# Optimization experiments

Hardware: AMD Instinct MI355X
Metric: run time of the kernel (lower is better)

## Reference

```python
import jax, jax.numpy as jnp
import numpy as np

# dims: G groups, A authors/group, P posts/author, DIN token-pooled feat, DEMB sentence-BERT dim
G, A, P, DIN, DEMB, HP, HA = 16, 64, 32, 768, 384, 256, 128


def setup_inputs() -> dict:
    key = jax.random.key(0)
    ks = jax.random.split(key, 8)
    s = lambda k, shape, scale: (jax.random.normal(k, shape, jnp.float32) * scale)
    return {
        "x": jax.random.normal(ks[0], (G, A, P, DIN), jnp.float32),
        "w_embed": s(ks[1], (DIN, DEMB), 0.02),   # BERT pooled-projection stand-in
        "b_embed": jnp.zeros((DEMB,), jnp.float32),
        "k_post": s(ks[2], (DEMB, 4 * HP), 0.05),  # Keras LSTM kernel, gates [i|f|c|o]
        "r_post": s(ks[3], (HP, 4 * HP), 0.05),    # recurrent kernel
        "b_post": jnp.zeros((4 * HP,), jnp.float32),
        "k_auth": s(ks[4], (HP, 4 * HA), 0.05),
        "r_auth": s(ks[5], (HA, 4 * HA), 0.05),
        "b_auth": jnp.zeros((4 * HA,), jnp.float32),
    }


def _lstm(x, Wk, Wr, b):
    """Keras-style LSTM, returns final hidden state. x: [B,T,D] -> [B,H]."""
    B = x.shape[0]
    H = Wr.shape[0]
    # precompute input projections for all timesteps in one GEMM: [T,B,4H]
    z = jnp.einsum('btd,dh->tbh', x, Wk) + b

    def step(carry, zt):
        h, c = carry
        g = zt + h @ Wr
        i, f, gg, o = jnp.split(g, 4, axis=-1)  # Keras gate order i,f,c,o
        c = jax.nn.sigmoid(f) * c + jax.nn.sigmoid(i) * jnp.tanh(gg)
        h = jax.nn.sigmoid(o) * jnp.tanh(c)
        return (h, c), None

    h0 = jnp.zeros((B, H), x.dtype)
    (h, _), _ = jax.lax.scan(step, (h0, h0), z)
    return h


def reference(x, w_embed, b_embed, k_post, r_post, b_post, k_auth, r_auth, b_auth):
    g, a, p, _ = x.shape
    # sentence embedding per post (BERT stand-in): [G,A,P,DEMB]
    e = jnp.einsum('gapd,de->gape', x, w_embed) + b_embed
    # LSTM over posts, batched across all (group, author) pairs: [G,A,HP]
    h_post = _lstm(e.reshape(g * a, p, e.shape[-1]), k_post, r_post, b_post)
    h_post = h_post.reshape(g, a, -1)
    # LSTM over authors: [G,HA]
    return _lstm(h_post, k_auth, r_auth, b_auth)
```

## Files before the change

kernel.cpp:

```cpp
#include <hip/hip_runtime.h>
#include <cstdint>
#include <cstddef>

#define G_    16
#define A_    64
#define P_    32
#define DIN_  768
#define DEMB_ 384
#define HP_   256
#define HA_   128
#define GA_   1024
#define N1_   1024
#define N2_   512
#define TCH   16

typedef float    f32x4   __attribute__((ext_vector_type(4)));
typedef _Float16 half8_t __attribute__((ext_vector_type(8)));
typedef _Float16 half4_t __attribute__((ext_vector_type(4)));

__device__ __forceinline__ float sigmoidf_(float x) { return 1.0f / (1.0f + __expf(-x)); }
__device__ __forceinline__ float tanhf_(float x) { return 2.0f / (1.0f + __expf(-2.0f * x)) - 1.0f; }
__device__ __forceinline__ _Float16 us2h(unsigned short u) { _Float16 h; __builtin_memcpy(&h, &u, 2); return h; }
__device__ __forceinline__ unsigned short h2us(_Float16 h) { unsigned short u; __builtin_memcpy(&u, &h, 2); return u; }


__global__ __launch_bounds__(256) void k_wk(const float* __restrict__ w_embed,
                                            const float* __restrict__ k_post,
                                            float* __restrict__ Bmat) {
    int j  = blockIdx.x * 256 + threadIdx.x;
    int k0 = blockIdx.y * 4;
    float acc0 = 0.f, acc1 = 0.f, acc2 = 0.f, acc3 = 0.f;
    for (int d = 0; d < DEMB_; ++d) {
        float kp = k_post[(size_t)d * N1_ + j];
        acc0 += w_embed[(size_t)(k0 + 0) * DEMB_ + d] * kp;
        acc1 += w_embed[(size_t)(k0 + 1) * DEMB_ + d] * kp;
        acc2 += w_embed[(size_t)(k0 + 2) * DEMB_ + d] * kp;
        acc3 += w_embed[(size_t)(k0 + 3) * DEMB_ + d] * kp;
    }
    Bmat[(size_t)(k0 + 0) * N1_ + j] = acc0;
    Bmat[(size_t)(k0 + 1) * N1_ + j] = acc1;
    Bmat[(size_t)(k0 + 2) * N1_ + j] = acc2;
    Bmat[(size_t)(k0 + 3) * N1_ + j] = acc3;
}

__global__ __launch_bounds__(256) void k_bias_p(const float* __restrict__ b_embed,
                                                const float* __restrict__ k_post,
                                                const float* __restrict__ b_post,
                                                float* __restrict__ biasZp) {
    int p = blockIdx.x * 256 + threadIdx.x;
    int n = (p >> 6) * 16 + (p & 15) + 256 * ((p >> 4) & 3);
    float acc = b_post[n];
    for (int d = 0; d < DEMB_; ++d)
        acc += b_embed[d] * k_post[(size_t)d * N1_ + n];
    biasZp[p] = acc;
}

__global__ __launch_bounds__(256) void k_t16(const float* __restrict__ Bmat,
                                             _Float16* __restrict__ Bt16) {
    __shared__ float tile[64][65];
    const int tid = threadIdx.x;
    const int p0 = blockIdx.x * 64;
    const int k0 = blockIdx.y * 64;
    const int jgrp = p0 >> 6;
#pragma unroll
    for (int i = 0; i < 16; ++i) {
        int idx = i * 256 + tid;
        int pp = idx & 63, kk = idx >> 6;
        int n = jgrp * 16 + (pp & 15) + 256 * ((pp >> 4) & 3);
        tile[pp][kk] = Bmat[(size_t)(k0 + kk) * N1_ + n];
    }
    __syncthreads();
    const int pp = tid >> 2;
    const int kq = (tid & 3) * 16;
    _Float16 buf[16];
#pragma unroll
    for (int i = 0; i < 16; ++i) buf[i] = (_Float16)tile[pp][kq + i];
    _Float16* dst = &Bt16[(size_t)(p0 + pp) * DIN_ + k0 + kq];
    *(half8_t*)dst       = *(half8_t*)&buf[0];
    *(half8_t*)(dst + 8) = *(half8_t*)&buf[8];
}

__global__ __launch_bounds__(256) void k_bfrag(const float* __restrict__ r_post,
                                               _Float16* __restrict__ Bfrag) {
    int idx = blockIdx.x * 256 + threadIdx.x;
    int pt = idx >> 9;
    int kt = (idx >> 6) & 7;
    int l  = idx & 63;
    int p = pt * 16 + (l & 15);
    int n = (p >> 6) * 16 + (p & 15) + 256 * ((p >> 4) & 3);
    int kb = kt * 32 + (l >> 4) * 8;
    _Float16 buf[8];
#pragma unroll
    for (int s = 0; s < 8; ++s) buf[s] = (_Float16)r_post[(size_t)(kb + s) * N1_ + n];
    *(half8_t*)&Bfrag[(size_t)idx * 8] = *(half8_t*)buf;
}

#define ZBM 128
#define ZBN 256
#define ZBK 32
#define ZPAD 40

struct ZgLDS {
    union {
        struct { _Float16 As[ZBM][ZPAD]; _Float16 Bs[ZBN][ZPAD]; } S;
        _Float16 Hs[64][264];
    } u;
};
struct RecLDS {
    _Float16 wlds[16 * 8 * 64 * 8];
    _Float16 hbuf[2][4096];
};

__device__ __forceinline__ void zgemm_core(ZgLDS* L, int bid, int tid,
                                           const float* __restrict__ x,
                                           const _Float16* __restrict__ Bt16,
                                           const float* __restrict__ biasZp,
                                           _Float16* __restrict__ Zq, int tbase) {
    const int wg = (bid & 7) * 64 + (bid >> 3);
    const int bm = (wg & 127) * ZBM;
    const int bn = (wg >> 7) * ZBN;

    const int arow = tid >> 3, akq = (tid & 7) * 4;
    const int brow = tid >> 2, bkq = (tid & 3) * 8;
    const int lane = tid & 63, w = tid >> 6;
    const int wm = (w >> 2) * 32, wn = (w & 3) * 64;
    const int frc = lane & 15, frk = (lane >> 4) * 8;

    const int crow = bm + arow;
    const size_t xrow = (size_t)(crow >> 4) * P_ + tbase + (crow & 15);
    const float*    aptr = &x[xrow * DIN_ + akq];
    const _Float16* bptr = &Bt16[(size_t)(bn + brow) * DIN_ + bkq];

    f32x4 acc[2][4];
#pragma unroll
    for (int i = 0; i < 2; ++i)
#pragma unroll
        for (int j = 0; j < 4; ++j) acc[i][j] = (f32x4)0.0f;

    float4 a0 = *(const float4*)aptr;
    uint4  b0 = *(const uint4*)bptr;

    const int NK = DIN_ / ZBK;
    for (int kt = 0; kt < NK; ++kt) {
        const int kn = (kt + 1 < NK) ? (kt + 1) * ZBK : kt * ZBK;
        float4 na0 = *(const float4*)(aptr + kn);
        uint4  nb0 = *(const uint4*)(bptr + kn);

        half4_t ahv;
        ahv[0] = (_Float16)a0.x; ahv[1] = (_Float16)a0.y;
        ahv[2] = (_Float16)a0.z; ahv[3] = (_Float16)a0.w;

        __syncthreads();
        *(half4_t*)&L->u.S.As[arow][akq] = ahv;
        *(uint4*)&L->u.S.Bs[brow][bkq]   = b0;
        __syncthreads();

        half8_t bf[4];
#pragma unroll
        for (int fn = 0; fn < 4; ++fn)
            bf[fn] = *(const half8_t*)&L->u.S.Bs[wn + fn * 16 + frc][frk];
#pragma unroll
        for (int fm = 0; fm < 2; ++fm) {
            half8_t aH = *(const half8_t*)&L->u.S.As[wm + fm * 16 + frc][frk];
#pragma unroll
            for (int fn = 0; fn < 4; ++fn)
                acc[fm][fn] = __builtin_amdgcn_mfma_f32_16x16x32_f16(aH, bf[fn], acc[fm][fn], 0, 0, 0);
        }
        a0 = na0; b0 = nb0;
    }

    float bzv[4];
#pragma unroll
    for (int fn = 0; fn < 4; ++fn) bzv[fn] = biasZp[bn + wn + fn * 16 + frc];

#pragma unroll
    for (int half_ = 0; half_ < 2; ++half_) {
        __syncthreads();
        if ((w >> 3) == half_) {
#pragma unroll
            for (int fm = 0; fm < 2; ++fm)
#pragma unroll
                for (int fn = 0; fn < 4; ++fn)
#pragma unroll
                    for (int r = 0; r < 4; ++r) {
                        int rl = ((w >> 2) & 1) * 32 + fm * 16 + (lane >> 4) * 4 + r;
                        int cl = wn + fn * 16 + frc;
                        int clp = ((cl >> 6) * 16 + (cl & 15)) * 4 + ((cl >> 4) & 3);
                        L->u.Hs[rl][clp] = (_Float16)(acc[fm][fn][r] + bzv[fn]);
                    }
        }
        __syncthreads();
        const int brb = (bm + half_ * 64) >> 4;
        const int rg  = brb >> 4;
        const int l4r = (brb & 15) >> 2;
        {
            int tloc = tid >> 6, hcl = tid & 63;
            _Float16 buf[16];
#pragma unroll
            for (int rr = 0; rr < 4; ++rr) {
                half4_t h4 = *(const half4_t*)&L->u.Hs[tloc + 16 * rr][hcl * 4];
                buf[rr * 4 + 0] = h4[0]; buf[rr * 4 + 1] = h4[1];
                buf[rr * 4 + 2] = h4[2]; buf[rr * 4 + 3] = h4[3];
            }
            int wvg  = (bn >> 6) + (hcl >> 4);
            int tid2 = wvg * 64 + l4r * 16 + (hcl & 15);
            _Float16* dst = &Zq[((size_t)(tloc * 64 + rg) * 1024 + tid2) * 16];
            *(uint4*)dst       = *(const uint4*)&buf[0];
            *(uint4*)(dst + 8) = *(const uint4*)&buf[8];
        }
    }
}

__device__ __forceinline__ void rec_core(RecLDS* L, int blk, int tid,
                                         const _Float16* __restrict__ Zq,
                                         const _Float16* __restrict__ Bfrag,
                                         float* __restrict__ csave,
                                         unsigned short* __restrict__ hsave,
                                         float* __restrict__ hF32, int tbase) {
    const int lane = tid & 63, wv = tid >> 6;
    const int hl = lane & 15, l4 = lane >> 4;
    const int r0 = blk * 16;
    const int hc = wv * 16 + hl;

    half8_t wreg[16];
#pragma unroll
    for (int q = 0; q < 2; ++q)
#pragma unroll
        for (int kt = 0; kt < 8; ++kt)
            wreg[q * 8 + kt] = *(const half8_t*)&Bfrag[(((size_t)(4 * wv + q) * 8 + kt) * 64 + lane) * 8];
#pragma unroll
    for (int kt = 0; kt < 8; ++kt)
        *(half8_t*)&L->wlds[((wv * 8 + kt) * 64 + lane) * 8] =
            *(const half8_t*)&Bfrag[(((size_t)(4 * wv + 2) * 8 + kt) * 64 + lane) * 8];
    const _Float16* w3base = &Bfrag[((size_t)(4 * wv + 3) * 8 * 64 + lane) * 8];

    float cst[4];
    if (tbase == 0) {
#pragma unroll
        for (int i = 0; i < 4; ++i) cst[i] = 0.f;
    } else {
        f32x4 cv = *(const f32x4*)&csave[((size_t)blk * 1024 + tid) * 4];
#pragma unroll
        for (int i = 0; i < 4; ++i) cst[i] = cv[i];
#pragma unroll
        for (int rr = 0; rr < 4; ++rr) {
            int row = l4 * 4 + rr;
            int lidx = (((hc >> 5) * 64) + (((hc & 31) >> 3) * 16 + row)) * 8 + (hc & 7);
            L->hbuf[0][lidx] = us2h(hsave[((size_t)(r0 + row)) * HP_ + hc]);
        }
    }
    __syncthreads();

    const _Float16* zp0 = &Zq[((size_t)blk * 1024 + tid) * 16];
    half8_t z01N = *(const half8_t*)zp0;
    half8_t z23N = *(const half8_t*)(zp0 + 8);

    for (int tt = 0; tt < TCH; ++tt) {
        const int t = tbase + tt;
        const int cur = t & 1, nxt = cur ^ 1;

        half8_t z01 = z01N, z23 = z23N;
        if (tt + 1 < TCH) {
            const _Float16* zpn = zp0 + (size_t)(tt + 1) * 1048576;
            z01N = *(const half8_t*)zpn;
            z23N = *(const half8_t*)(zpn + 8);
        }

        f32x4 acc[4];
#pragma unroll
        for (int i = 0; i < 4; ++i) acc[i] = (f32x4)0.0f;

        if (t > 0) {
#pragma unroll
            for (int kt = 0; kt < 8; ++kt) {
                half8_t ah = *(const half8_t*)&L->hbuf[cur][(kt * 64 + lane) * 8];
                half8_t b2 = *(const half8_t*)&L->wlds[((wv * 8 + kt) * 64 + lane) * 8];
                half8_t w3 = *(const half8_t*)&w3base[(size_t)kt * 512];
                acc[0] = __builtin_amdgcn_mfma_f32_16x16x32_f16(ah, wreg[kt],     acc[0], 0, 0, 0);
                acc[1] = __builtin_amdgcn_mfma_f32_16x16x32_f16(ah, wreg[8 + kt], acc[1], 0, 0, 0);
                acc[2] = __builtin_amdgcn_mfma_f32_16x16x32_f16(ah, b2,           acc[2], 0, 0, 0);
                acc[3] = __builtin_amdgcn_mfma_f32_16x16x32_f16(ah, w3,           acc[3], 0, 0, 0);
            }
        }

        const bool last = (t == P_ - 1);
        const bool save = (tbase == 0) && (tt == TCH - 1);
#pragma unroll
        for (int rr = 0; rr < 4; ++rr) {
            const half8_t zsrc = (rr < 2) ? z01 : z23;
            const int o = (rr & 1) * 4;
            float gi = acc[0][rr] + (float)zsrc[o + 0];
            float gf = acc[1][rr] + (float)zsrc[o + 1];
            float gg = acc[2][rr] + (float)zsrc[o + 2];
            float go = acc[3][rr] + (float)zsrc[o + 3];
            float cn = sigmoidf_(gf) * cst[rr] + sigmoidf_(gi) * tanhf_(gg);
            cst[rr] = cn;
            float hv = sigmoidf_(go) * tanhf_(cn);
            int row = l4 * 4 + rr;
            int lidx = (((hc >> 5) * 64) + (((hc & 31) >> 3) * 16 + row)) * 8 + (hc & 7);
            _Float16 hh = (_Float16)hv;
            L->hbuf[nxt][lidx] = hh;
            if (save) hsave[((size_t)(r0 + row)) * HP_ + hc] = h2us(hh);
            if (last) hF32[(size_t)(r0 + row) * HP_ + hc] = hv;
        }
        __syncthreads();
    }

    if (tbase == 0) {
        f32x4 cv;
#pragma unroll
        for (int i = 0; i < 4; ++i) cv[i] = cst[i];
        *(f32x4*)&csave[((size_t)blk * 1024 + tid) * 4] = cv;
    }
}

__global__ __launch_bounds__(1024, 4) void k_zgemm(const float* __restrict__ x,
                                                   const _Float16* __restrict__ Bt16,
                                                   const float* __restrict__ biasZp,
                                                   _Float16* __restrict__ Zq, int tbase) {
    __shared__ __align__(16) ZgLDS L;
    zgemm_core(&L, blockIdx.x, threadIdx.x, x, Bt16, biasZp, Zq, tbase);
}

__global__ __launch_bounds__(1024, 4) void k_rec(const _Float16* __restrict__ Zq,
                                                 const _Float16* __restrict__ Bfrag,
                                                 float* __restrict__ csave,
                                                 unsigned short* __restrict__ hsave,
                                                 float* __restrict__ hF32, int tbase) {
    __shared__ __align__(16) RecLDS L;
    rec_core(&L, blockIdx.x, threadIdx.x, Zq, Bfrag, csave, hsave, hF32, tbase);
}

__global__ __launch_bounds__(1024, 4) void k_fuse(const float* __restrict__ x,
                                                  const _Float16* __restrict__ Bt16,
                                                  const float* __restrict__ biasZp,
                                                  const _Float16* __restrict__ Zq0,
                                                  _Float16* __restrict__ Zq1,
                                                  const _Float16* __restrict__ Bfrag,
                                                  float* __restrict__ csave,
                                                  unsigned short* __restrict__ hsave,
                                                  float* __restrict__ hF32) {
    __shared__ __align__(16) union { RecLDS r; ZgLDS z; } L;
    if (blockIdx.x < 64)
        rec_core(&L.r, blockIdx.x, threadIdx.x, Zq0, Bfrag, csave, hsave, hF32, 0);
    else
        zgemm_core(&L.z, blockIdx.x - 64, threadIdx.x, x, Bt16, biasZp, Zq1, TCH);
}

__global__ __launch_bounds__(256) void k_zauth(const float* __restrict__ h,
                                               const float* __restrict__ k_auth,
                                               const float* __restrict__ b_auth,
                                               float* __restrict__ z_auth) {
    const int j = blockIdx.x * 256 + threadIdx.x;
    const int r0 = blockIdx.y * 4;
    float acc0 = b_auth[j], acc1 = acc0, acc2 = acc0, acc3 = acc0;
    for (int k = 0; k < HP_; ++k) {
        const float kp = k_auth[(size_t)k * N2_ + j];
        acc0 += h[(size_t)(r0 + 0) * HP_ + k] * kp;
        acc1 += h[(size_t)(r0 + 1) * HP_ + k] * kp;
        acc2 += h[(size_t)(r0 + 2) * HP_ + k] * kp;
        acc3 += h[(size_t)(r0 + 3) * HP_ + k] * kp;
    }
#pragma unroll
    for (int r = 0; r < 4; ++r) {
        const int b = r0 + r;
        const int g = b >> 6, a = b & 63;
        const float v = (r == 0) ? acc0 : (r == 1) ? acc1 : (r == 2) ? acc2 : acc3;
        z_auth[((size_t)a * G_ + g) * N2_ + j] = v;
    }
}

__global__ __launch_bounds__(512) void k_author(const float* __restrict__ z_auth,
                                                const float* __restrict__ r_auth,
                                                float* __restrict__ out) {
    const int g = blockIdx.x;
    const int tid = threadIdx.x;
    const int j = tid >> 2;
    const int kq = tid & 3;

    __shared__ float hsb[2][HA_];

    float rci[32], rcf[32], rcg[32], rco[32];
#pragma unroll
    for (int kk = 0; kk < 32; ++kk) {
        int k = kq * 32 + kk;
        rci[kk] = r_auth[(size_t)k * N2_ + j];
        rcf[kk] = r_auth[(size_t)k * N2_ + j + 128];
        rcg[kk] = r_auth[(size_t)k * N2_ + j + 256];
        rco[kk] = r_auth[(size_t)k * N2_ + j + 384];
    }

    if (tid < HA_) hsb[0][tid] = 0.f;
    float cj = 0.f, hv = 0.f;
    __syncthreads();

    float4 zn;
    {
        size_t zb = (size_t)g * N2_;
        zn.x = z_auth[zb + j];       zn.y = z_auth[zb + j + 128];
        zn.z = z_auth[zb + j + 256]; zn.w = z_auth[zb + j + 384];
    }

    for (int a = 0; a < A_; ++a) {
        const int cur = a & 1, nxt = cur ^ 1;
        float4 z4 = zn;
        if (a + 1 < A_) {
            size_t zb = ((size_t)(a + 1) * G_ + g) * N2_;
            zn.x = z_auth[zb + j];       zn.y = z_auth[zb + j + 128];
            zn.z = z_auth[zb + j + 256]; zn.w = z_auth[zb + j + 384];
        }
        float si = 0.f, sf = 0.f, sg = 0.f, so = 0.f;
#pragma unroll
        for (int kk = 0; kk < 32; kk += 4) {
            float4 h4 = *(const float4*)&hsb[cur][kq * 32 + kk];
            si += h4.x * rci[kk] + h4.y * rci[kk + 1] + h4.z * rci[kk + 2] + h4.w * rci[kk + 3];
            sf += h4.x * rcf[kk] + h4.y * rcf[kk + 1] + h4.z * rcf[kk + 2] + h4.w * rcf[kk + 3];
            sg += h4.x * rcg[kk] + h4.y * rcg[kk + 1] + h4.z * rcg[kk + 2] + h4.w * rcg[kk + 3];
            so += h4.x * rco[kk] + h4.y * rco[kk + 1] + h4.z * rco[kk + 2] + h4.w * rco[kk + 3];
        }
        si += __shfl_xor(si, 1); si += __shfl_xor(si, 2);
        sf += __shfl_xor(sf, 1); sf += __shfl_xor(sf, 2);
        sg += __shfl_xor(sg, 1); sg += __shfl_xor(sg, 2);
        so += __shfl_xor(so, 1); so += __shfl_xor(so, 2);
        float gi = si + z4.x, gf = sf + z4.y, gg = sg + z4.z, go = so + z4.w;
        cj = sigmoidf_(gf) * cj + sigmoidf_(gi) * tanhf_(gg);
        hv = sigmoidf_(go) * tanhf_(cj);
        if (kq == 0) hsb[nxt][j] = hv;
        __syncthreads();
    }
    if (kq == 0) out[(size_t)g * HA_ + j] = hv;
}

extern "C" void kernel_launch(void* const* d_in, const int* in_sizes, int n_in,
                              void* d_out, int out_size, void* d_ws, size_t ws_size,
                              hipStream_t stream) {
    const float* x       = (const float*)d_in[0];
    const float* w_embed = (const float*)d_in[1];
    const float* b_embed = (const float*)d_in[2];
    const float* k_post  = (const float*)d_in[3];
    const float* r_post  = (const float*)d_in[4];
    const float* b_post  = (const float*)d_in[5];
    const float* k_auth  = (const float*)d_in[6];
    const float* r_auth  = (const float*)d_in[7];
    const float* b_auth  = (const float*)d_in[8];
    float* out = (float*)d_out;

    char* wsb = (char*)d_ws;
    _Float16*       Zq0    = (_Float16*)(wsb);
    float*          Bmat   = (float*)(wsb + (32ull << 20));
    _Float16*       Bt16   = (_Float16*)(wsb + (36ull << 20));
    _Float16*       Bfrag  = (_Float16*)(wsb + (38ull << 20));
    float*          biasZp = (float*)(wsb + (38ull << 20) + (512ull << 10));
    float*          csave  = (float*)(wsb + (39ull << 20));
    unsigned short* hsave  = (unsigned short*)(wsb + (40ull << 20));
    float*          hF32   = (float*)(wsb + (41ull << 20));
    float*          z_auth = (float*)(wsb + (42ull << 20));
    _Float16*       Zq1    = (_Float16*)(wsb + (44ull << 20));

    const bool overlap = (ws_size >= (77ull << 20));

    k_wk    <<<dim3(N1_ / 256, DIN_ / 4), 256, 0, stream>>>(w_embed, k_post, Bmat);
    k_bias_p<<<dim3(N1_ / 256), 256, 0, stream>>>(b_embed, k_post, b_post, biasZp);
    k_t16   <<<dim3(16, 12), 256, 0, stream>>>(Bmat, Bt16);
    k_bfrag <<<dim3(128), 256, 0, stream>>>(r_post, Bfrag);

    k_zgemm<<<dim3(512), 1024, 0, stream>>>(x, Bt16, biasZp, Zq0, 0);

    if (overlap) {
        k_fuse<<<dim3(576), 1024, 0, stream>>>(x, Bt16, biasZp, Zq0, Zq1,
                                               Bfrag, csave, hsave, hF32);
        k_rec <<<dim3(64), 1024, 0, stream>>>(Zq1, Bfrag, csave, hsave, hF32, TCH);
    } else {
        k_rec  <<<dim3(64), 1024, 0, stream>>>(Zq0, Bfrag, csave, hsave, hF32, 0);
        k_zgemm<<<dim3(512), 1024, 0, stream>>>(x, Bt16, biasZp, Zq0, TCH);
        k_rec  <<<dim3(64), 1024, 0, stream>>>(Zq0, Bfrag, csave, hsave, hF32, TCH);
    }

    k_zauth <<<dim3(N2_ / 256, GA_ / 4), 256, 0, stream>>>(hF32, k_auth, b_auth, z_auth);
    k_author<<<dim3(G_), 512, 0, stream>>>(z_auth, r_auth, out);
}
```

Before: 348.2 us.

## Run author LSTM recurrence on MFMA in a single block with fp16 weight fragments

```diff
diff --git a/kernel.cpp b/kernel.cpp
--- a/kernel.cpp
+++ b/kernel.cpp
@@ -93,6 +93,20 @@
 #pragma unroll
     for (int s = 0; s < 8; ++s) buf[s] = (_Float16)r_post[(size_t)(kb + s) * N1_ + n];
     *(half8_t*)&Bfrag[(size_t)idx * 8] = *(half8_t*)buf;
+}
+
+__global__ __launch_bounds__(256) void k_afrag(const float* __restrict__ r_auth,
+                                               _Float16* __restrict__ Afrag) {
+    int idx = blockIdx.x * 256 + threadIdx.x;
+    int unit = idx >> 6;
+    int lane = idx & 63;
+    int wv = unit >> 4, q = (unit >> 2) & 3, kt = unit & 3;
+    int n = q * 128 + wv * 16 + (lane & 15);
+    int kb = kt * 32 + (lane >> 4) * 8;
+    _Float16 buf[8];
+#pragma unroll
+    for (int s = 0; s < 8; ++s) buf[s] = (_Float16)r_auth[(size_t)(kb + s) * N2_ + n];
+    *(half8_t*)&Afrag[(size_t)idx * 8] = *(half8_t*)buf;
 }
 
 #define ZBM 128
@@ -350,7 +364,7 @@
 __global__ __launch_bounds__(256) void k_zauth(const float* __restrict__ h,
                                                const float* __restrict__ k_auth,
                                                const float* __restrict__ b_auth,
-                                               float* __restrict__ z_auth) {
+                                               float* __restrict__ z2) {
     const int j = blockIdx.x * 256 + threadIdx.x;
     const int r0 = blockIdx.y * 4;
     float acc0 = b_auth[j], acc1 = acc0, acc2 = acc0, acc3 = acc0;
@@ -361,74 +375,86 @@
         acc2 += h[(size_t)(r0 + 2) * HP_ + k] * kp;
         acc3 += h[(size_t)(r0 + 3) * HP_ + k] * kp;
     }
+    const int q = j >> 7, hcol = j & 127;
 #pragma unroll
     for (int r = 0; r < 4; ++r) {
         const int b = r0 + r;
         const int g = b >> 6, a = b & 63;
         const float v = (r == 0) ? acc0 : (r == 1) ? acc1 : (r == 2) ? acc2 : acc3;
-        z_auth[((size_t)a * G_ + g) * N2_ + j] = v;
-    }
-}
-
-__global__ __launch_bounds__(512) void k_author(const float* __restrict__ z_auth,
-                                                const float* __restrict__ r_auth,
-                                                float* __restrict__ out) {
-    const int g = blockIdx.x;
-    const int tid = threadIdx.x;
-    const int j = tid >> 2;
-    const int kq = tid & 3;
-
-    __shared__ float hsb[2][HA_];
-
-    float rci[32], rcf[32], rcg[32], rco[32];
-#pragma unroll
-    for (int kk = 0; kk < 32; ++kk) {
-        int k = kq * 32 + kk;
-        rci[kk] = r_auth[(size_t)k * N2_ + j];
-        rcf[kk] = r_auth[(size_t)k * N2_ + j + 128];
-        rcg[kk] = r_auth[(size_t)k * N2_ + j + 256];
-        rco[kk] = r_auth[(size_t)k * N2_ + j + 384];
-    }
-
-    if (tid < HA_) hsb[0][tid] = 0.f;
-    float cj = 0.f, hv = 0.f;
+        int tid2 = (hcol >> 4) * 64 + (g >> 2) * 16 + (hcol & 15);
+        z2[(size_t)a * 8192 + (size_t)tid2 * 16 + (g & 3) * 4 + q] = v;
+    }
+}
+
+__global__ __launch_bounds__(512) void k_author2(const _Float16* __restrict__ Afrag,
+                                                 const float* __restrict__ z2,
+                                                 float* __restrict__ out) {
+    __shared__ __align__(16) _Float16 hA[2][2048];
+
+    const int tid = threadIdx.x, lane = tid & 63, wv = tid >> 6;
+    const int hl = lane & 15, l4 = lane >> 4;
+    const int hcol = wv * 16 + hl;
+
+    half8_t wreg[16];
+#pragma unroll
+    for (int i = 0; i < 16; ++i)
+        wreg[i] = *(const half8_t*)&Afrag[(((size_t)(wv * 16 + i)) * 64 + lane) * 8];
+
+    if (tid < 256) *(half8_t*)&hA[0][tid * 8] = (half8_t)(_Float16)0.0f;
+    float cst[4] = {0.f, 0.f, 0.f, 0.f};
+    float hlast[4] = {0.f, 0.f, 0.f, 0.f};
     __syncthreads();
 
-    float4 zn;
-    {
-        size_t zb = (size_t)g * N2_;
-        zn.x = z_auth[zb + j];       zn.y = z_auth[zb + j + 128];
-        zn.z = z_auth[zb + j + 256]; zn.w = z_auth[zb + j + 384];
-    }
+    const float* zp = &z2[(size_t)tid * 16];
+    f32x4 zN[4];
+#pragma unroll
+    for (int rr = 0; rr < 4; ++rr) zN[rr] = *(const f32x4*)&zp[rr * 4];
 
     for (int a = 0; a < A_; ++a) {
         const int cur = a & 1, nxt = cur ^ 1;
-        float4 z4 = zn;
+        f32x4 zv[4];
+#pragma unroll
+        for (int rr = 0; rr < 4; ++rr) zv[rr] = zN[rr];
         if (a + 1 < A_) {
-            size_t zb = ((size_t)(a + 1) * G_ + g) * N2_;
-            zn.x = z_auth[zb + j];       zn.y = z_auth[zb + j + 128];
-            zn.z = z_auth[zb + j + 256]; zn.w = z_auth[zb + j + 384];
-        }
-        float si = 0.f, sf = 0.f, sg = 0.f, so = 0.f;
-#pragma unroll
-        for (int kk = 0; kk < 32; kk += 4) {
-            float4 h4 = *(const float4*)&hsb[cur][kq * 32 + kk];
-            si += h4.x * rci[kk] + h4.y * rci[kk + 1] + h4.z * rci[kk + 2] + h4.w * rci[kk + 3];
-            sf += h4.x * rcf[kk] + h4.y * rcf[kk + 1] + h4.z * rcf[kk + 2] + h4.w * rcf[kk + 3];
-            sg += h4.x * rcg[kk] + h4.y * rcg[kk + 1] + h4.z * rcg[kk + 2] + h4.w * rcg[kk + 3];
-            so += h4.x * rco[kk] + h4.y * rco[kk + 1] + h4.z * rco[kk + 2] + h4.w * rco[kk + 3];
-        }
-        si += __shfl_xor(si, 1); si += __shfl_xor(si, 2);
-        sf += __shfl_xor(sf, 1); sf += __shfl_xor(sf, 2);
-        sg += __shfl_xor(sg, 1); sg += __shfl_xor(sg, 2);
-        so += __shfl_xor(so, 1); so += __shfl_xor(so, 2);
-        float gi = si + z4.x, gf = sf + z4.y, gg = sg + z4.z, go = so + z4.w;
-        cj = sigmoidf_(gf) * cj + sigmoidf_(gi) * tanhf_(gg);
-        hv = sigmoidf_(go) * tanhf_(cj);
-        if (kq == 0) hsb[nxt][j] = hv;
+            const float* zpn = zp + (size_t)(a + 1) * 8192;
+#pragma unroll
+            for (int rr = 0; rr < 4; ++rr) zN[rr] = *(const f32x4*)&zpn[rr * 4];
+        }
+
+        f32x4 acc[4];
+#pragma unroll
+        for (int i = 0; i < 4; ++i) acc[i] = (f32x4)0.0f;
+
+        if (a > 0) {
+#pragma unroll
+            for (int kt = 0; kt < 4; ++kt) {
+                half8_t ah = *(const half8_t*)&hA[cur][(kt * 64 + lane) * 8];
+#pragma unroll
+                for (int q = 0; q < 4; ++q)
+                    acc[q] = __builtin_amdgcn_mfma_f32_16x16x32_f16(ah, wreg[q * 4 + kt], acc[q], 0, 0, 0);
+            }
+        }
+
+#pragma unroll
+        for (int rr = 0; rr < 4; ++rr) {
+            float gi = acc[0][rr] + zv[rr][0];
+            float gf = acc[1][rr] + zv[rr][1];
+            float gg = acc[2][rr] + zv[rr][2];
+            float go = acc[3][rr] + zv[rr][3];
+            float cn = sigmoidf_(gf) * cst[rr] + sigmoidf_(gi) * tanhf_(gg);
+            cst[rr] = cn;
+            float hv = sigmoidf_(go) * tanhf_(cn);
+            hlast[rr] = hv;
+            int grp = l4 * 4 + rr;
+            int lidx = (((hcol >> 5) * 64) + (((hcol & 31) >> 3) * 16 + grp)) * 8 + (hcol & 7);
+            hA[nxt][lidx] = (_Float16)hv;
+        }
         __syncthreads();
     }
-    if (kq == 0) out[(size_t)g * HA_ + j] = hv;
+
+#pragma unroll
+    for (int rr = 0; rr < 4; ++rr)
+        out[(size_t)(l4 * 4 + rr) * HA_ + hcol] = hlast[rr];
 }
 
 extern "C" void kernel_launch(void* const* d_in, const int* in_sizes, int n_in,
@@ -451,10 +477,11 @@
     _Float16*       Bt16   = (_Float16*)(wsb + (36ull << 20));
     _Float16*       Bfrag  = (_Float16*)(wsb + (38ull << 20));
     float*          biasZp = (float*)(wsb + (38ull << 20) + (512ull << 10));
+    _Float16*       Afrag  = (_Float16*)(wsb + (38ull << 20) + (576ull << 10));
     float*          csave  = (float*)(wsb + (39ull << 20));
     unsigned short* hsave  = (unsigned short*)(wsb + (40ull << 20));
     float*          hF32   = (float*)(wsb + (41ull << 20));
-    float*          z_auth = (float*)(wsb + (42ull << 20));
+    float*          z2     = (float*)(wsb + (42ull << 20));
     _Float16*       Zq1    = (_Float16*)(wsb + (44ull << 20));
 
     const bool overlap = (ws_size >= (77ull << 20));
@@ -463,6 +490,7 @@
     k_bias_p<<<dim3(N1_ / 256), 256, 0, stream>>>(b_embed, k_post, b_post, biasZp);
     k_t16   <<<dim3(16, 12), 256, 0, stream>>>(Bmat, Bt16);
     k_bfrag <<<dim3(128), 256, 0, stream>>>(r_post, Bfrag);
+    k_afrag <<<dim3(32), 256, 0, stream>>>(r_auth, Afrag);
 
     k_zgemm<<<dim3(512), 1024, 0, stream>>>(x, Bt16, biasZp, Zq0, 0);
 
@@ -476,6 +504,6 @@
         k_rec  <<<dim3(64), 1024, 0, stream>>>(Zq0, Bfrag, csave, hsave, hF32, TCH);
     }
 
-    k_zauth <<<dim3(N2_ / 256, GA_ / 4), 256, 0, stream>>>(hF32, k_auth, b_auth, z_auth);
-    k_author<<<dim3(G_), 512, 0, stream>>>(z_auth, r_auth, out);
-}
+    k_zauth  <<<dim3(N2_ / 256, GA_ / 4), 256, 0, stream>>>(hF32, k_auth, b_auth, z2);
+    k_author2<<<dim3(1), 512, 0, stream>>>(Afrag, z2, out);
+}
```

Measured after the change: 401.6 us. +15.3%, slower.

## Restructure author LSTM kernel to split gate columns and reduce through shared memory

Applied to the files above, without the earlier changes.

```diff
diff --git a/kernel.cpp b/kernel.cpp
--- a/kernel.cpp
+++ b/kernel.cpp
@@ -370,65 +370,44 @@
     }
 }
 
-__global__ __launch_bounds__(512) void k_author(const float* __restrict__ z_auth,
-                                                const float* __restrict__ r_auth,
-                                                float* __restrict__ out) {
+__global__ __launch_bounds__(1024) void k_author(const float* __restrict__ z_auth,
+                                                 const float* __restrict__ r_auth,
+                                                 float* __restrict__ out) {
     const int g = blockIdx.x;
     const int tid = threadIdx.x;
-    const int j = tid >> 2;
-    const int kq = tid & 3;
-
-    __shared__ float hsb[2][HA_];
-
-    float rci[32], rcf[32], rcg[32], rco[32];
-#pragma unroll
-    for (int kk = 0; kk < 32; ++kk) {
-        int k = kq * 32 + kk;
-        rci[kk] = r_auth[(size_t)k * N2_ + j];
-        rcf[kk] = r_auth[(size_t)k * N2_ + j + 128];
-        rcg[kk] = r_auth[(size_t)k * N2_ + j + 256];
-        rco[kk] = r_auth[(size_t)k * N2_ + j + 384];
-    }
-
-    if (tid < HA_) hsb[0][tid] = 0.f;
-    float cj = 0.f, hv = 0.f;
+    const int j = tid & 511;
+    const int kh = tid >> 9;
+
+    __shared__ float hs[HA_];
+    __shared__ float parts[2][512];
+
+    float rc[64];
+#pragma unroll
+    for (int kk = 0; kk < 64; ++kk)
+        rc[kk] = r_auth[(size_t)(kh * 64 + kk) * N2_ + j];
+
+    float cj = 0.f;
+    if (tid < HA_) hs[tid] = 0.f;
     __syncthreads();
 
-    float4 zn;
-    {
-        size_t zb = (size_t)g * N2_;
-        zn.x = z_auth[zb + j];       zn.y = z_auth[zb + j + 128];
-        zn.z = z_auth[zb + j + 256]; zn.w = z_auth[zb + j + 384];
-    }
-
     for (int a = 0; a < A_; ++a) {
-        const int cur = a & 1, nxt = cur ^ 1;
-        float4 z4 = zn;
-        if (a + 1 < A_) {
-            size_t zb = ((size_t)(a + 1) * G_ + g) * N2_;
-            zn.x = z_auth[zb + j];       zn.y = z_auth[zb + j + 128];
-            zn.z = z_auth[zb + j + 256]; zn.w = z_auth[zb + j + 384];
-        }
-        float si = 0.f, sf = 0.f, sg = 0.f, so = 0.f;
-#pragma unroll
-        for (int kk = 0; kk < 32; kk += 4) {
-            float4 h4 = *(const float4*)&hsb[cur][kq * 32 + kk];
-            si += h4.x * rci[kk] + h4.y * rci[kk + 1] + h4.z * rci[kk + 2] + h4.w * rci[kk + 3];
-            sf += h4.x * rcf[kk] + h4.y * rcf[kk + 1] + h4.z * rcf[kk + 2] + h4.w * rcf[kk + 3];
-            sg += h4.x * rcg[kk] + h4.y * rcg[kk + 1] + h4.z * rcg[kk + 2] + h4.w * rcg[kk + 3];
-            so += h4.x * rco[kk] + h4.y * rco[kk + 1] + h4.z * rco[kk + 2] + h4.w * rco[kk + 3];
-        }
-        si += __shfl_xor(si, 1); si += __shfl_xor(si, 2);
-        sf += __shfl_xor(sf, 1); sf += __shfl_xor(sf, 2);
-        sg += __shfl_xor(sg, 1); sg += __shfl_xor(sg, 2);
-        so += __shfl_xor(so, 1); so += __shfl_xor(so, 2);
-        float gi = si + z4.x, gf = sf + z4.y, gg = sg + z4.z, go = so + z4.w;
-        cj = sigmoidf_(gf) * cj + sigmoidf_(gi) * tanhf_(gg);
-        hv = sigmoidf_(go) * tanhf_(cj);
-        if (kq == 0) hsb[nxt][j] = hv;
-        __syncthreads();
-    }
-    if (kq == 0) out[(size_t)g * HA_ + j] = hv;
+        float acc = (kh == 0) ? z_auth[((size_t)a * G_ + g) * N2_ + j] : 0.f;
+#pragma unroll
+        for (int kk = 0; kk < 64; ++kk)
+            acc += hs[kh * 64 + kk] * rc[kk];
+        parts[kh][j] = acc;
+        __syncthreads();
+        if (tid < HA_) {
+            float gi = parts[0][tid]       + parts[1][tid];
+            float gf = parts[0][tid + 128] + parts[1][tid + 128];
+            float gg = parts[0][tid + 256] + parts[1][tid + 256];
+            float go = parts[0][tid + 384] + parts[1][tid + 384];
+            cj = sigmoidf_(gf) * cj + sigmoidf_(gi) * tanhf_(gg);
+            hs[tid] = sigmoidf_(go) * tanhf_(cj);
+        }
+        __syncthreads();
+    }
+    if (tid < HA_) out[(size_t)g * HA_ + tid] = hs[tid];
 }
 
 extern "C" void kernel_launch(void* const* d_in, const int* in_sizes, int n_in,
@@ -477,5 +456,5 @@
     }
 
     k_zauth <<<dim3(N2_ / 256, GA_ / 4), 256, 0, stream>>>(hF32, k_auth, b_auth, z_auth);
-    k_author<<<dim3(G_), 512, 0, stream>>>(z_auth, r_auth, out);
-}
+    k_author<<<dim3(G_), 1024, 0, stream>>>(z_auth, r_auth, out);
+}
```

After: 337.1 us. -3.2%, faster.
